# Kernel tuning notes

Hardware: AMD Instinct MI355X
Metric: run time of the kernel (lower is better)

Reference implementation:

```python
import jax, jax.numpy as jnp
import numpy as np

N_STATE = 1024
N_HEAD = 16
HEAD_DIM = N_STATE // N_HEAD


def setup_inputs() -> dict:
    key = jax.random.key(0)
    ks = jax.random.split(key, 8)
    B, S = 8, 1500
    x = jax.random.normal(ks[0], (B, S, N_STATE), dtype=jnp.float32)
    # additive causal mask (0 on/below diagonal, -inf above), broadcast over B,H
    neg = jnp.float32(-1e9)
    mask = jnp.where(jnp.tril(jnp.ones((S, S), dtype=bool)), 0.0, neg).astype(jnp.float32)
    s = 0.02
    Wq = jax.random.normal(ks[1], (N_STATE, N_STATE), dtype=jnp.float32) * s
    bq = jnp.zeros((N_STATE,), dtype=jnp.float32)
    Wk = jax.random.normal(ks[2], (N_STATE, N_STATE), dtype=jnp.float32) * s
    Wv = jax.random.normal(ks[3], (N_STATE, N_STATE), dtype=jnp.float32) * s
    bv = jnp.zeros((N_STATE,), dtype=jnp.float32)
    Wo = jax.random.normal(ks[4], (N_STATE, N_STATE), dtype=jnp.float32) * s
    bo = jnp.zeros((N_STATE,), dtype=jnp.float32)
    return {"x": x, "mask": mask, "Wq": Wq, "bq": bq, "Wk": Wk, "Wv": Wv, "bv": bv, "Wo": Wo, "bo": bo}


def reference(x, mask, Wq, bq, Wk, Wv, bv, Wo, bo):
    B, S, _ = x.shape
    # linear projections (torch Linear: x @ W^T + b); W stored as [out, in]
    q = x @ Wq.T + bq
    k = x @ Wk.T
    v = x @ Wv.T + bv
    # [B, H, S, D]
    q = q.reshape(B, S, N_HEAD, HEAD_DIM).transpose(0, 2, 1, 3)
    k = k.reshape(B, S, N_HEAD, HEAD_DIM).transpose(0, 2, 1, 3)
    v = v.reshape(B, S, N_HEAD, HEAD_DIM).transpose(0, 2, 1, 3)
    scale = 1.0 / np.sqrt(HEAD_DIM).astype(np.float32)
    scores = jnp.einsum('bhqd,bhkd->bhqk', q, k) * scale + mask
    attn = jax.nn.softmax(scores, axis=-1)
    out = jnp.einsum('bhqk,bhkd->bhqd', attn, v)
    out = out.transpose(0, 2, 1, 3).reshape(B, S, N_STATE)
    return out @ Wo.T + bo
```

## Files before the change

kernel.cpp:

```cpp
#include <hip/hip_runtime.h>
#include <hip/hip_bf16.h>

#define N_STATE 1024
#define N_HEAD  16
#define D_HEAD  64
#define BATCH   8
#define SEQ     1500
#define ROWS    (BATCH*SEQ)
#define SVP     1536
#define MTILES  94

#define BM 128
#define BN 128
#define BK 32
#define BK2 64

typedef __bf16 bf16x8 __attribute__((ext_vector_type(8)));
typedef __bf16 bf16x4 __attribute__((ext_vector_type(4)));
typedef float  f32x4  __attribute__((ext_vector_type(4)));

__device__ __forceinline__ f32x4 mfma16(bf16x8 a, bf16x8 b, f32x4 c) {
  return __builtin_amdgcn_mfma_f32_16x16x32_bf16(a, b, c, 0, 0, 0);
}

__device__ __forceinline__ void gl_lds16(const void* g, void* l) {
  __builtin_amdgcn_global_load_lds(
      (const __attribute__((address_space(1))) unsigned int*)g,
      (__attribute__((address_space(3))) unsigned int*)l, 16, 0, 0);
}

__global__ __launch_bounds__(256)
void cvt_all(const float* __restrict__ x,  const float* __restrict__ wq,
             const float* __restrict__ wk, const float* __restrict__ wv,
             const float* __restrict__ wo,
             __bf16* __restrict__ xb, __bf16* __restrict__ wb)
{
  const int which = blockIdx.y;
  const float* src;
  __bf16* dst;
  size_t n;
  if (which == 0) { src = x; dst = xb; n = (size_t)ROWS * N_STATE; }
  else {
    src = (which == 1) ? wq : (which == 2) ? wk : (which == 3) ? wv : wo;
    dst = wb + (size_t)(which - 1) * N_STATE * N_STATE;
    n = (size_t)N_STATE * N_STATE;
  }
  const size_t stride = (size_t)gridDim.x * 256 * 4;
  for (size_t i = ((size_t)blockIdx.x * 256 + threadIdx.x) * 4; i < n; i += stride) {
    const f32x4 v = *(const f32x4*)(src + i);
    bf16x4 c; c[0]=(__bf16)v[0]; c[1]=(__bf16)v[1]; c[2]=(__bf16)v[2]; c[3]=(__bf16)v[3];
    *(bf16x4*)(dst + i) = c;
  }
}

__global__ __launch_bounds__(256)
void qkv_fast(const __bf16* __restrict__ xb, const __bf16* __restrict__ wb,
              const float* __restrict__ bq, const float* __restrict__ bv,
              __bf16* __restrict__ q_ws, __bf16* __restrict__ k_ws,
              __bf16* __restrict__ vt_ws)
{
  const int xcd = blockIdx.x & 7;
  const int jj  = blockIdx.x >> 3;
  const int nt  = jj & 7;
  const int mt  = (jj >> 3) * 8 + xcd;
  if (mt >= MTILES) return;

  __shared__ __bf16 lA[BM * BK2];
  __shared__ __bf16 lB[BN * BK2];
  const int which = blockIdx.z;
  const __bf16* W = wb + (size_t)which * N_STATE * N_STATE;

  const int tid = threadIdx.x;
  const int lane = tid & 63, wave = tid >> 6;
  const int l15 = lane & 15, quad = lane >> 4;
  const int wr = wave >> 1, wc = wave & 1;

  f32x4 acc[4][4] = {};

  for (int k0 = 0; k0 < N_STATE; k0 += BK2) {
#pragma unroll
    for (int t = 0; t < 4; ++t) {
      const int c = wave * 4 + t;
      const int s = c * 64 + lane;
      const int row = s >> 3;
      const int sw  = (lane & 7) ^ (row & 7);
      const int ga = min(mt * BM + row, ROWS - 1);
      gl_lds16(xb + (size_t)ga * N_STATE + k0 + sw * 8, (__bf16*)lA + c * 512);
      const int gb = nt * BN + row;
      gl_lds16(W + (size_t)gb * N_STATE + k0 + sw * 8, (__bf16*)lB + c * 512);
    }
    __syncthreads();
#pragma unroll
    for (int h = 0; h < 2; ++h) {
      bf16x8 af[4], bfr[4];
#pragma unroll
      for (int i = 0; i < 4; ++i) {
        const int ra = wr * 64 + i * 16 + l15;
        const int rb = wc * 64 + i * 16 + l15;
        af[i]  = *(const bf16x8*)&lA[ra * BK2 + (((h * 4 + quad) ^ (ra & 7)) * 8)];
        bfr[i] = *(const bf16x8*)&lB[rb * BK2 + (((h * 4 + quad) ^ (rb & 7)) * 8)];
      }
      if (which != 2) {
#pragma unroll
        for (int i = 0; i < 4; ++i)
#pragma unroll
          for (int j = 0; j < 4; ++j)
            acc[i][j] = mfma16(af[i], bfr[j], acc[i][j]);
      } else {
#pragma unroll
        for (int i = 0; i < 4; ++i)
#pragma unroll
          for (int j = 0; j < 4; ++j)
            acc[i][j] = mfma16(bfr[j], af[i], acc[i][j]);
      }
    }
    __syncthreads();
  }

  if (which != 2) {
#pragma unroll
    for (int i = 0; i < 4; ++i) {
      const int mrow = mt * BM + wr * 64 + i * 16 + quad * 4;
#pragma unroll
      for (int j = 0; j < 4; ++j) {
        const int col = nt * BN + wc * 64 + j * 16 + l15;
        const int h = col >> 6, d = col & 63;
        const float badd = (which == 0) ? bq[col] : 0.0f;
        __bf16* dst = (which == 0) ? q_ws : k_ws;
#pragma unroll
        for (int r = 0; r < 4; ++r) {
          const int row = mrow + r;
          if (row < ROWS) {
            const int b = row / SEQ, s = row % SEQ;
            dst[(((size_t)(b * N_HEAD + h)) * SEQ + s) * D_HEAD + d] =
                (__bf16)(acc[i][j][r] + badd);
          }
        }
      }
    }
  } else {
#pragma unroll
    for (int i = 0; i < 4; ++i) {
      const int sg = mt * BM + wr * 64 + i * 16 + l15;
      const bool valid = sg < ROWS;
      const int b = sg / SEQ, srow = sg % SEQ;
#pragma unroll
      for (int j = 0; j < 4; ++j) {
        const int dbase = nt * BN + wc * 64 + j * 16 + quad * 4;
#pragma unroll
        for (int r = 0; r < 4; ++r) {
          const int d = dbase + r;
          const int h = d >> 6, dd = d & 63;
          if (valid)
            vt_ws[(((size_t)(b * N_HEAD + h)) * D_HEAD + dd) * SVP + srow] =
                (__bf16)(acc[i][j][r] + bv[d]);
        }
      }
    }
  }
}

__global__ __launch_bounds__(256)
void out_fast(const __bf16* __restrict__ a_in, const __bf16* __restrict__ wob,
              const float* __restrict__ bo, float* __restrict__ out)
{
  const int xcd = blockIdx.x & 7;
  const int jj  = blockIdx.x >> 3;
  const int nt  = jj & 7;
  const int mt  = (jj >> 3) * 8 + xcd;
  if (mt >= MTILES) return;

  __shared__ __bf16 lA[BM * BK2];
  __shared__ __bf16 lB[BN * BK2];
  const int tid = threadIdx.x;
  const int lane = tid & 63, wave = tid >> 6;
  const int l15 = lane & 15, quad = lane >> 4;
  const int wr = wave >> 1, wc = wave & 1;

  f32x4 acc[4][4] = {};

  for (int k0 = 0; k0 < N_STATE; k0 += BK2) {
#pragma unroll
    for (int t = 0; t < 4; ++t) {
      const int c = wave * 4 + t;
      const int s = c * 64 + lane;
      const int row = s >> 3;
      const int sw  = (lane & 7) ^ (row & 7);
      const int ga = min(mt * BM + row, ROWS - 1);
      gl_lds16(a_in + (size_t)ga * N_STATE + k0 + sw * 8, (__bf16*)lA + c * 512);
      const int gb = nt * BN + row;
      gl_lds16(wob + (size_t)gb * N_STATE + k0 + sw * 8, (__bf16*)lB + c * 512);
    }
    __syncthreads();
#pragma unroll
    for (int h = 0; h < 2; ++h) {
      bf16x8 af[4], bfr[4];
#pragma unroll
      for (int i = 0; i < 4; ++i) {
        const int ra = wr * 64 + i * 16 + l15;
        const int rb = wc * 64 + i * 16 + l15;
        af[i]  = *(const bf16x8*)&lA[ra * BK2 + (((h * 4 + quad) ^ (ra & 7)) * 8)];
        bfr[i] = *(const bf16x8*)&lB[rb * BK2 + (((h * 4 + quad) ^ (rb & 7)) * 8)];
      }
#pragma unroll
      for (int i = 0; i < 4; ++i)
#pragma unroll
        for (int j = 0; j < 4; ++j)
          acc[i][j] = mfma16(af[i], bfr[j], acc[i][j]);
    }
    __syncthreads();
  }

#pragma unroll
  for (int i = 0; i < 4; ++i) {
    const int mrow = mt * BM + wr * 64 + i * 16 + quad * 4;
#pragma unroll
    for (int j = 0; j < 4; ++j) {
      const int col = nt * BN + wc * 64 + j * 16 + l15;
      const float badd = bo[col];
#pragma unroll
      for (int r = 0; r < 4; ++r) {
        const int row = mrow + r;
        if (row < ROWS)
          out[(size_t)row * N_STATE + col] = acc[i][j][r] + badd;
      }
    }
  }
}

__global__ __launch_bounds__(256)
void qkv_gemm(const float* __restrict__ x,
              const float* __restrict__ Wq, const float* __restrict__ bq,
              const float* __restrict__ Wk,
              const float* __restrict__ Wv, const float* __restrict__ bv,
              __bf16* __restrict__ q_ws, __bf16* __restrict__ k_ws,
              __bf16* __restrict__ vt_ws)
{
  __shared__ __bf16 lA[BM * BK];
  __shared__ __bf16 lB[BN * BK];
  const int which = blockIdx.z;
  const float* W    = (which == 0) ? Wq : (which == 1) ? Wk : Wv;
  const float* bias = (which == 0) ? bq : (which == 2) ? bv : nullptr;

  const int mt = blockIdx.x, nt = blockIdx.y;
  const int tid = threadIdx.x;
  const int lane = tid & 63, wave = tid >> 6;
  const int l15 = lane & 15, quad = lane >> 4;
  const int wr = wave >> 1, wc = wave & 1;

  f32x4 acc[4][4] = {};

  for (int k0 = 0; k0 < N_STATE; k0 += BK) {
#pragma unroll
    for (int it = 0; it < 4; ++it) {
      const int s = tid + it * 256;
      const int row = s >> 3, seg = s & 7;
      const int ga = min(mt * BM + row, ROWS - 1);
      const f32x4 va = *(const f32x4*)(x + (size_t)ga * N_STATE + k0 + seg * 4);
      bf16x4 ca; ca[0]=(__bf16)va[0]; ca[1]=(__bf16)va[1];
                 ca[2]=(__bf16)va[2]; ca[3]=(__bf16)va[3];
      *(bf16x4*)&lA[row * BK + seg * 4] = ca;
      const int gb = nt * BM + row;
      const f32x4 vb = *(const f32x4*)(W + (size_t)gb * N_STATE + k0 + seg * 4);
      bf16x4 cb; cb[0]=(__bf16)vb[0]; cb[1]=(__bf16)vb[1];
                 cb[2]=(__bf16)vb[2]; cb[3]=(__bf16)vb[3];
      *(bf16x4*)&lB[row * BK + seg * 4] = cb;
    }
    __syncthreads();
    bf16x8 af[4], bfr[4];
#pragma unroll
    for (int i = 0; i < 4; ++i) {
      af[i]  = *(const bf16x8*)&lA[(wr * 64 + i * 16 + l15) * BK + quad * 8];
      bfr[i] = *(const bf16x8*)&lB[(wc * 64 + i * 16 + l15) * BK + quad * 8];
    }
    if (which != 2) {
#pragma unroll
      for (int i = 0; i < 4; ++i)
#pragma unroll
        for (int j = 0; j < 4; ++j)
          acc[i][j] = mfma16(af[i], bfr[j], acc[i][j]);
    } else {
#pragma unroll
      for (int i = 0; i < 4; ++i)
#pragma unroll
        for (int j = 0; j < 4; ++j)
          acc[i][j] = mfma16(bfr[j], af[i], acc[i][j]);
    }
    __syncthreads();
  }

  if (which != 2) {
#pragma unroll
    for (int i = 0; i < 4; ++i) {
      const int mrow = mt * BM + wr * 64 + i * 16 + quad * 4;
#pragma unroll
      for (int j = 0; j < 4; ++j) {
        const int col = nt * BN + wc * 64 + j * 16 + l15;
        const int h = col >> 6, d = col & 63;
        const float badd = bias ? bias[col] : 0.0f;
        __bf16* dst = (which == 0) ? q_ws : k_ws;
#pragma unroll
        for (int r = 0; r < 4; ++r) {
          const int row = mrow + r;
          if (row < ROWS) {
            const int b = row / SEQ, s = row % SEQ;
            dst[(((size_t)(b * N_HEAD + h)) * SEQ + s) * D_HEAD + d] =
                (__bf16)(acc[i][j][r] + badd);
          }
        }
      }
    }
  } else {
#pragma unroll
    for (int i = 0; i < 4; ++i) {
      const int sg = mt * BM + wr * 64 + i * 16 + l15;
      const bool valid = sg < ROWS;
      const int b = sg / SEQ, srow = sg % SEQ;
#pragma unroll
      for (int j = 0; j < 4; ++j) {
        const int dbase = nt * BN + wc * 64 + j * 16 + quad * 4;
#pragma unroll
        for (int r = 0; r < 4; ++r) {
          const int d = dbase + r;
          const int h = d >> 6, dd = d & 63;
          if (valid)
            vt_ws[(((size_t)(b * N_HEAD + h)) * D_HEAD + dd) * SVP + srow] =
                (__bf16)(acc[i][j][r] + bias[d]);
        }
      }
    }
  }
}

__global__ __launch_bounds__(256)
void flash_attn(const __bf16* __restrict__ q_ws, const __bf16* __restrict__ k_ws,
                const __bf16* __restrict__ vt_ws, __bf16* __restrict__ attn)
{
  __shared__ __align__(16) __bf16 lK[8 * 512];
  __shared__ __align__(16) __bf16 lV[8 * 512];
  __shared__ __align__(16) __bf16 lP[4 * 16 * 72];
  const int bh = blockIdx.x;
  const int qt = gridDim.y - 1 - blockIdx.y;
  const int tid = threadIdx.x, lane = tid & 63, wave = tid >> 6;
  const int l15 = lane & 15, quad = lane >> 4;
  const __bf16* Q  = q_ws  + (size_t)bh * SEQ * D_HEAD;
  const __bf16* K  = k_ws  + (size_t)bh * SEQ * D_HEAD;
  const __bf16* Vt = vt_ws + (size_t)bh * D_HEAD * SVP;
  __bf16* lPw = lP + wave * 16 * 72;

  const int q0 = qt * 64, wq0 = q0 + wave * 16;
  const int qload = min(wq0 + l15, SEQ - 1);
  const bf16x8 qa0 = *(const bf16x8*)(Q + (size_t)qload * D_HEAD + quad * 8);
  const bf16x8 qa1 = *(const bf16x8*)(Q + (size_t)qload * D_HEAD + 32 + quad * 8);

  const float NEG = -1.0e30f;
  const float scale = 0.125f;
  const int query = wq0 + l15;
  f32x4 o[4] = {};
  float m_i = NEG, l_i = 0.0f;

  const int kmax = min(q0 + 63, SEQ - 1);
  const int wqmax = wq0 + 15;

  for (int kt = 0; kt <= kmax; kt += 64) {
#pragma unroll
    for (int t = 0; t < 2; ++t) {
      const int c = wave * 2 + t;
      const int gk = min(kt + lane, SEQ - 1);
      gl_lds16(K + (size_t)gk * D_HEAD + c * 8, (__bf16*)lK + c * 512);
      gl_lds16(Vt + (size_t)lane * SVP + kt + c * 8, (__bf16*)lV + c * 512);
    }
    __syncthreads();

    if (kt <= wqmax) {
      f32x4 sg[4] = {};
#pragma unroll
      for (int g = 0; g < 4; ++g) {
        const bf16x8 k0 = *(const bf16x8*)&lK[quad * 512 + (g * 16 + l15) * 8];
        const bf16x8 k1 = *(const bf16x8*)&lK[(4 + quad) * 512 + (g * 16 + l15) * 8];
        sg[g] = mfma16(k0, qa0, sg[g]);
        sg[g] = mfma16(k1, qa1, sg[g]);
      }
      const bool fullvis = (kt + 63 <= wq0) && (kt + 63 < SEQ);
      float tmax = NEG;
#pragma unroll
      for (int g = 0; g < 4; ++g)
#pragma unroll
        for (int r = 0; r < 4; ++r) {
          float v = sg[g][r] * scale;
          if (!fullvis) {
            const int key = kt + g * 16 + quad * 4 + r;
            v = (key <= query && key < SEQ) ? v : NEG;
          }
          sg[g][r] = v;
          tmax = fmaxf(tmax, v);
        }
      tmax = fmaxf(tmax, __shfl_xor(tmax, 16));
      tmax = fmaxf(tmax, __shfl_xor(tmax, 32));
      const float mnew = fmaxf(m_i, tmax);
      const float alpha = __expf(m_i - mnew);
      float rsum = 0.0f;
#pragma unroll
      for (int g = 0; g < 4; ++g) {
        bf16x4 pk;
#pragma unroll
        for (int r = 0; r < 4; ++r) {
          const float e = __expf(sg[g][r] - mnew);
          rsum += e;
          pk[r] = (__bf16)e;
        }
        *(bf16x4*)&lPw[l15 * 72 + g * 16 + quad * 4] = pk;
      }
      rsum += __shfl_xor(rsum, 16);
      rsum += __shfl_xor(rsum, 32);
      l_i = l_i * alpha + rsum;
      m_i = mnew;
#pragma unroll
      for (int nn = 0; nn < 4; ++nn)
#pragma unroll
        for (int r = 0; r < 4; ++r) o[nn][r] *= alpha;

#pragma unroll
      for (int h = 0; h < 2; ++h) {
        const bf16x8 pb = *(const bf16x8*)&lPw[l15 * 72 + h * 32 + quad * 8];
#pragma unroll
        for (int nn = 0; nn < 4; ++nn) {
          const bf16x8 va =
              *(const bf16x8*)&lV[(h * 4 + quad) * 512 + (nn * 16 + l15) * 8];
          o[nn] = mfma16(va, pb, o[nn]);
        }
      }
    }
    __syncthreads();
  }

  const int b = bh >> 4, hh = bh & 15;
  if (query < SEQ) {
    const float inv = 1.0f / l_i;
#pragma unroll
    for (int nn = 0; nn < 4; ++nn) {
      bf16x4 ov;
#pragma unroll
      for (int r = 0; r < 4; ++r) ov[r] = (__bf16)(o[nn][r] * inv);
      *(bf16x4*)&attn[(((size_t)(b * SEQ + query)) * N_HEAD + hh) * D_HEAD +
                      nn * 16 + quad * 4] = ov;
    }
  }
}

__global__ __launch_bounds__(256)
void out_gemm(const __bf16* __restrict__ a_in, const float* __restrict__ Wo,
              const float* __restrict__ bo, float* __restrict__ out)
{
  __shared__ __bf16 lA[BM * BK];
  __shared__ __bf16 lB[BN * BK];
  const int mt = blockIdx.x, nt = blockIdx.y;
  const int tid = threadIdx.x;
  const int lane = tid & 63, wave = tid >> 6;
  const int l15 = lane & 15, quad = lane >> 4;
  const int wr = wave >> 1, wc = wave & 1;

  f32x4 acc[4][4] = {};

  for (int k0 = 0; k0 < N_STATE; k0 += BK) {
#pragma unroll
    for (int it = 0; it < 2; ++it) {
      const int s = tid + it * 256;
      const int row = s >> 2, seg = s & 3;
      const int ga = min(mt * BM + row, ROWS - 1);
      *(bf16x8*)&lA[row * BK + seg * 8] =
          *(const bf16x8*)(a_in + (size_t)ga * N_STATE + k0 + seg * 8);
    }
#pragma unroll
    for (int it = 0; it < 4; ++it) {
      const int s = tid + it * 256;
      const int row = s >> 3, seg = s & 7;
      const int gb = nt * BM + row;
      const f32x4 vb = *(const f32x4*)(Wo + (size_t)gb * N_STATE + k0 + seg * 4);
      bf16x4 cb; cb[0]=(__bf16)vb[0]; cb[1]=(__bf16)vb[1];
                 cb[2]=(__bf16)vb[2]; cb[3]=(__bf16)vb[3];
      *(bf16x4*)&lB[row * BK + seg * 4] = cb;
    }
    __syncthreads();
    bf16x8 af[4], bfr[4];
#pragma unroll
    for (int i = 0; i < 4; ++i) {
      af[i]  = *(const bf16x8*)&lA[(wr * 64 + i * 16 + l15) * BK + quad * 8];
      bfr[i] = *(const bf16x8*)&lB[(wc * 64 + i * 16 + l15) * BK + quad * 8];
    }
#pragma unroll
    for (int i = 0; i < 4; ++i)
#pragma unroll
      for (int j = 0; j < 4; ++j)
        acc[i][j] = mfma16(af[i], bfr[j], acc[i][j]);
    __syncthreads();
  }

#pragma unroll
  for (int i = 0; i < 4; ++i) {
    const int mrow = mt * BM + wr * 64 + i * 16 + quad * 4;
#pragma unroll
    for (int j = 0; j < 4; ++j) {
      const int col = nt * BN + wc * 64 + j * 16 + l15;
      const float badd = bo[col];
#pragma unroll
      for (int r = 0; r < 4; ++r) {
        const int row = mrow + r;
        if (row < ROWS)
          out[(size_t)row * N_STATE + col] = acc[i][j][r] + badd;
      }
    }
  }
}

extern "C" void kernel_launch(void* const* d_in, const int* in_sizes, int n_in,
                              void* d_out, int out_size, void* d_ws, size_t ws_size,
                              hipStream_t stream) {
  const float* x  = (const float*)d_in[0];
  const float* Wq = (const float*)d_in[2];
  const float* bq = (const float*)d_in[3];
  const float* Wk = (const float*)d_in[4];
  const float* Wv = (const float*)d_in[5];
  const float* bv = (const float*)d_in[6];
  const float* Wo = (const float*)d_in[7];
  const float* bo = (const float*)d_in[8];
  float* out = (float*)d_out;

  const size_t chunk  = (size_t)ROWS * N_STATE;
  const size_t vchunk = (size_t)BATCH * N_HEAD * D_HEAD * SVP;
  const size_t wchunk = (size_t)4 * N_STATE * N_STATE;
  __bf16* q_ws  = (__bf16*)d_ws;
  __bf16* k_ws  = q_ws + chunk;
  __bf16* vt_ws = k_ws + chunk;
  __bf16* attn  = vt_ws + vchunk;
  __bf16* xb    = attn;
  __bf16* wb    = attn + chunk;
  const size_t need = (3 * chunk + vchunk + wchunk) * sizeof(__bf16);

  const int MT = (ROWS + BM - 1) / BM;
  if (ws_size >= need) {
    cvt_all<<<dim3(1024, 5), 256, 0, stream>>>(x, Wq, Wk, Wv, Wo, xb, wb);
    qkv_fast<<<dim3(768, 1, 3), 256, 0, stream>>>(
        xb, wb, bq, bv, q_ws, k_ws, vt_ws);
    flash_attn<<<dim3(BATCH * N_HEAD, (SEQ + 63) / 64), 256, 0, stream>>>(
        q_ws, k_ws, vt_ws, attn);
    out_fast<<<dim3(768, 1, 1), 256, 0, stream>>>(
        attn, wb + (size_t)3 * N_STATE * N_STATE, bo, out);
  } else {
    qkv_gemm<<<dim3(MT, N_STATE / BN, 3), 256, 0, stream>>>(
        x, Wq, bq, Wk, Wv, bv, q_ws, k_ws, vt_ws);
    flash_attn<<<dim3(BATCH * N_HEAD, (SEQ + 63) / 64), 256, 0, stream>>>(
        q_ws, k_ws, vt_ws, attn);
    out_gemm<<<dim3(MT, N_STATE / BN), 256, 0, stream>>>(attn, Wo, bo, out);
  }
}
```

Baseline: 373.3 us.

## Process two 64-query sub-tiles per flash attention block to reuse K/V tiles

Each flash attention block now handles 128 queries: every wave keeps two 16-row query groups with separate online-softmax state and output accumulators. Each K/V tile loaded into shared memory is reused for both groups, roughly halving global K/V traffic and barrier count per query. The trade-off is half as many blocks (12 query tiles instead of 24 per head), higher register pressure from doubled accumulators, and coarser causal load balance.

```diff
diff --git a/kernel.cpp b/kernel.cpp
--- a/kernel.cpp
+++ b/kernel.cpp
@@ -348,19 +348,25 @@
   const __bf16* Vt = vt_ws + (size_t)bh * D_HEAD * SVP;
   __bf16* lPw = lP + wave * 16 * 72;
 
-  const int q0 = qt * 64, wq0 = q0 + wave * 16;
-  const int qload = min(wq0 + l15, SEQ - 1);
-  const bf16x8 qa0 = *(const bf16x8*)(Q + (size_t)qload * D_HEAD + quad * 8);
-  const bf16x8 qa1 = *(const bf16x8*)(Q + (size_t)qload * D_HEAD + 32 + quad * 8);
-
+  const int q0 = qt * 128;
   const float NEG = -1.0e30f;
   const float scale = 0.125f;
-  const int query = wq0 + l15;
-  f32x4 o[4] = {};
-  float m_i = NEG, l_i = 0.0f;
-
-  const int kmax = min(q0 + 63, SEQ - 1);
-  const int wqmax = wq0 + 15;
+
+  int wq0[2], query[2];
+  bf16x8 qa[2][2];
+  f32x4 o[2][4] = {};
+  float m_i[2], l_i[2];
+#pragma unroll
+  for (int s = 0; s < 2; ++s) {
+    wq0[s] = q0 + s * 64 + wave * 16;
+    query[s] = wq0[s] + l15;
+    const int qload = min(query[s], SEQ - 1);
+    qa[s][0] = *(const bf16x8*)(Q + (size_t)qload * D_HEAD + quad * 8);
+    qa[s][1] = *(const bf16x8*)(Q + (size_t)qload * D_HEAD + 32 + quad * 8);
+    m_i[s] = NEG; l_i[s] = 0.0f;
+  }
+
+  const int kmax = min(q0 + 127, SEQ - 1);
 
   for (int kt = 0; kt <= kmax; kt += 64) {
 #pragma unroll
@@ -372,62 +378,65 @@
     }
     __syncthreads();
 
-    if (kt <= wqmax) {
-      f32x4 sg[4] = {};
-#pragma unroll
-      for (int g = 0; g < 4; ++g) {
-        const bf16x8 k0 = *(const bf16x8*)&lK[quad * 512 + (g * 16 + l15) * 8];
-        const bf16x8 k1 = *(const bf16x8*)&lK[(4 + quad) * 512 + (g * 16 + l15) * 8];
-        sg[g] = mfma16(k0, qa0, sg[g]);
-        sg[g] = mfma16(k1, qa1, sg[g]);
-      }
-      const bool fullvis = (kt + 63 <= wq0) && (kt + 63 < SEQ);
-      float tmax = NEG;
-#pragma unroll
-      for (int g = 0; g < 4; ++g)
-#pragma unroll
-        for (int r = 0; r < 4; ++r) {
-          float v = sg[g][r] * scale;
-          if (!fullvis) {
-            const int key = kt + g * 16 + quad * 4 + r;
-            v = (key <= query && key < SEQ) ? v : NEG;
+#pragma unroll
+    for (int s = 0; s < 2; ++s) {
+      if (kt <= wq0[s] + 15) {
+        f32x4 sg[4] = {};
+#pragma unroll
+        for (int g = 0; g < 4; ++g) {
+          const bf16x8 k0 = *(const bf16x8*)&lK[quad * 512 + (g * 16 + l15) * 8];
+          const bf16x8 k1 = *(const bf16x8*)&lK[(4 + quad) * 512 + (g * 16 + l15) * 8];
+          sg[g] = mfma16(k0, qa[s][0], sg[g]);
+          sg[g] = mfma16(k1, qa[s][1], sg[g]);
+        }
+        const bool fullvis = (kt + 63 <= wq0[s]) && (kt + 63 < SEQ);
+        float tmax = NEG;
+#pragma unroll
+        for (int g = 0; g < 4; ++g)
+#pragma unroll
+          for (int r = 0; r < 4; ++r) {
+            float v = sg[g][r] * scale;
+            if (!fullvis) {
+              const int key = kt + g * 16 + quad * 4 + r;
+              v = (key <= query[s] && key < SEQ) ? v : NEG;
+            }
+            sg[g][r] = v;
+            tmax = fmaxf(tmax, v);
           }
-          sg[g][r] = v;
-          tmax = fmaxf(tmax, v);
-        }
-      tmax = fmaxf(tmax, __shfl_xor(tmax, 16));
-      tmax = fmaxf(tmax, __shfl_xor(tmax, 32));
-      const float mnew = fmaxf(m_i, tmax);
-      const float alpha = __expf(m_i - mnew);
-      float rsum = 0.0f;
-#pragma unroll
-      for (int g = 0; g < 4; ++g) {
-        bf16x4 pk;
-#pragma unroll
-        for (int r = 0; r < 4; ++r) {
-          const float e = __expf(sg[g][r] - mnew);
-          rsum += e;
-          pk[r] = (__bf16)e;
-        }
-        *(bf16x4*)&lPw[l15 * 72 + g * 16 + quad * 4] = pk;
-      }
-      rsum += __shfl_xor(rsum, 16);
-      rsum += __shfl_xor(rsum, 32);
-      l_i = l_i * alpha + rsum;
-      m_i = mnew;
-#pragma unroll
-      for (int nn = 0; nn < 4; ++nn)
-#pragma unroll
-        for (int r = 0; r < 4; ++r) o[nn][r] *= alpha;
-
-#pragma unroll
-      for (int h = 0; h < 2; ++h) {
-        const bf16x8 pb = *(const bf16x8*)&lPw[l15 * 72 + h * 32 + quad * 8];
-#pragma unroll
-        for (int nn = 0; nn < 4; ++nn) {
-          const bf16x8 va =
-              *(const bf16x8*)&lV[(h * 4 + quad) * 512 + (nn * 16 + l15) * 8];
-          o[nn] = mfma16(va, pb, o[nn]);
+        tmax = fmaxf(tmax, __shfl_xor(tmax, 16));
+        tmax = fmaxf(tmax, __shfl_xor(tmax, 32));
+        const float mnew = fmaxf(m_i[s], tmax);
+        const float alpha = __expf(m_i[s] - mnew);
+        float rsum = 0.0f;
+#pragma unroll
+        for (int g = 0; g < 4; ++g) {
+          bf16x4 pk;
+#pragma unroll
+          for (int r = 0; r < 4; ++r) {
+            const float e = __expf(sg[g][r] - mnew);
+            rsum += e;
+            pk[r] = (__bf16)e;
+          }
+          *(bf16x4*)&lPw[l15 * 72 + g * 16 + quad * 4] = pk;
+        }
+        rsum += __shfl_xor(rsum, 16);
+        rsum += __shfl_xor(rsum, 32);
+        l_i[s] = l_i[s] * alpha + rsum;
+        m_i[s] = mnew;
+#pragma unroll
+        for (int nn = 0; nn < 4; ++nn)
+#pragma unroll
+          for (int r = 0; r < 4; ++r) o[s][nn][r] *= alpha;
+
+#pragma unroll
+        for (int h = 0; h < 2; ++h) {
+          const bf16x8 pb = *(const bf16x8*)&lPw[l15 * 72 + h * 32 + quad * 8];
+#pragma unroll
+          for (int nn = 0; nn < 4; ++nn) {
+            const bf16x8 va =
+                *(const bf16x8*)&lV[(h * 4 + quad) * 512 + (nn * 16 + l15) * 8];
+            o[s][nn] = mfma16(va, pb, o[s][nn]);
+          }
         }
       }
     }
@@ -435,15 +444,18 @@
   }
 
   const int b = bh >> 4, hh = bh & 15;
-  if (query < SEQ) {
-    const float inv = 1.0f / l_i;
-#pragma unroll
-    for (int nn = 0; nn < 4; ++nn) {
-      bf16x4 ov;
-#pragma unroll
-      for (int r = 0; r < 4; ++r) ov[r] = (__bf16)(o[nn][r] * inv);
-      *(bf16x4*)&attn[(((size_t)(b * SEQ + query)) * N_HEAD + hh) * D_HEAD +
-                      nn * 16 + quad * 4] = ov;
+#pragma unroll
+  for (int s = 0; s < 2; ++s) {
+    if (query[s] < SEQ) {
+      const float inv = 1.0f / l_i[s];
+#pragma unroll
+      for (int nn = 0; nn < 4; ++nn) {
+        bf16x4 ov;
+#pragma unroll
+        for (int r = 0; r < 4; ++r) ov[r] = (__bf16)(o[s][nn][r] * inv);
+        *(bf16x4*)&attn[(((size_t)(b * SEQ + query[s])) * N_HEAD + hh) * D_HEAD +
+                        nn * 16 + quad * 4] = ov;
+      }
     }
   }
 }
@@ -542,14 +554,14 @@
     cvt_all<<<dim3(1024, 5), 256, 0, stream>>>(x, Wq, Wk, Wv, Wo, xb, wb);
     qkv_fast<<<dim3(768, 1, 3), 256, 0, stream>>>(
         xb, wb, bq, bv, q_ws, k_ws, vt_ws);
-    flash_attn<<<dim3(BATCH * N_HEAD, (SEQ + 63) / 64), 256, 0, stream>>>(
+    flash_attn<<<dim3(BATCH * N_HEAD, (SEQ + 127) / 128), 256, 0, stream>>>(
         q_ws, k_ws, vt_ws, attn);
     out_fast<<<dim3(768, 1, 1), 256, 0, stream>>>(
         attn, wb + (size_t)3 * N_STATE * N_STATE, bo, out);
   } else {
     qkv_gemm<<<dim3(MT, N_STATE / BN, 3), 256, 0, stream>>>(
         x, Wq, bq, Wk, Wv, bv, q_ws, k_ws, vt_ws);
-    flash_attn<<<dim3(BATCH * N_HEAD, (SEQ + 63) / 64), 256, 0, stream>>>(
+    flash_attn<<<dim3(BATCH * N_HEAD, (SEQ + 127) / 128), 256, 0, stream>>>(
         q_ws, k_ws, vt_ws, attn);
     out_gemm<<<dim3(MT, N_STATE / BN), 256, 0, stream>>>(attn, Wo, bo, out);
   }
```

Measured after the change: 377.8 us. No clear change (+1.2%).
